# Performance work log

Measured on AMD Instinct MI355X. Metric: run time of the kernel, lower is better.

Reference implementation:

```python
import jax, jax.numpy as jnp
import numpy as np
from jax import lax

B, N, NUM_CLS_P1, MASK_DIM, PH, PW = 2, 19248, 81, 32, 138, 138
MAX_OUT, MAX_CLS_OUT = 300, 100
IOU_THR, SCORE_THR, SIGMA = 0.5, 0.3, 0.5


def setup_inputs() -> dict:
    key = jax.random.key(0)
    k1, k2, k3, k4, k5 = jax.random.split(key, 5)
    pred_offset = jax.random.normal(k1, (B, N, 4), jnp.float32) * 0.05
    # scale logits so softmax produces a realistic spread of scores above 0.3
    pred_cls = jax.random.normal(k2, (B, N, NUM_CLS_P1), jnp.float32) * 3.0
    pred_mask_coef = jax.random.normal(k3, (B, N, MASK_DIM), jnp.float32)
    pr = jax.random.uniform(k4, (N, 4), jnp.float32)
    ctr, wh = pr[:, :2], 0.05 + 0.2 * pr[:, 2:]
    priors = jnp.concatenate([ctr - wh / 2, ctr + wh / 2], axis=-1)  # [N,4] y1x1y2x2-ish
    proto_out = jax.random.normal(k5, (B, PH, PW, MASK_DIM), jnp.float32)
    return dict(pred_offset=pred_offset, pred_cls=pred_cls,
                pred_mask_coef=pred_mask_coef, priors=priors, proto_out=proto_out)


def _corners(b):
    # TF NMS normalizes unordered corners with min/max
    y1 = jnp.minimum(b[..., 0], b[..., 2]); y2 = jnp.maximum(b[..., 0], b[..., 2])
    x1 = jnp.minimum(b[..., 1], b[..., 3]); x2 = jnp.maximum(b[..., 1], b[..., 3])
    return y1, x1, y2, x2


def soft_nms(boxes, scores):
    # boxes [N,4], scores [N] -> (idx [K], score [K], valid [K]); valid is a prefix mask
    y1, x1, y2, x2 = _corners(boxes)
    area = (y2 - y1) * (x2 - x1)

    def step(s, _):
        i = jnp.argmax(s)
        sc = s[i]
        valid = sc > SCORE_THR  # TF NMSv5 selects strictly above score_threshold
        iy1 = jnp.maximum(y1, y1[i]); ix1 = jnp.maximum(x1, x1[i])
        iy2 = jnp.minimum(y2, y2[i]); ix2 = jnp.minimum(x2, x2[i])
        inter = jnp.maximum(iy2 - iy1, 0.0) * jnp.maximum(ix2 - ix1, 0.0)
        union = area + area[i] - inter
        iou = jnp.where((area > 0.0) & (area[i] > 0.0),
                        inter / jnp.where(union > 0.0, union, 1.0), 0.0)
        # Gaussian soft suppression below hard IoU threshold, hard zero above (TF semantics)
        w = jnp.where(iou <= IOU_THR, jnp.exp((-0.5 / SIGMA) * iou * iou), 0.0)
        s_new = (s * w).at[i].set(-jnp.inf)
        s_next = jnp.where(valid, s_new, s)  # freeze once below threshold (selection stops)
        return s_next, (i, sc, valid)

    _, (idx, sc, valid) = lax.scan(step, scores, None, length=MAX_CLS_OUT)
    return idx, sc, valid


def detect_one(boxes, cls_scores, coefs, proto):
    # boxes [N,4], cls_scores [N,C], coefs [N,D], proto [H,W,D]
    C = cls_scores.shape[1]
    idx, sc, valid = jax.vmap(lambda s: soft_nms(boxes, s))(cls_scores.T)  # [C,K]
    vf = valid.astype(boxes.dtype)
    sel_boxes = boxes[idx] * vf[..., None]                          # [C,K,4]
    sel_coefs = coefs[idx] * vf[..., None]                          # [C,K,D]
    sel_scores = jnp.where(valid, sc, 0.0)                          # [C,K]
    sel_classes = jnp.where(valid, jnp.arange(1, C + 1, dtype=boxes.dtype)[:, None], 0.0)
    flat_scores = sel_scores.reshape(-1)
    order = jnp.argsort(-flat_scores)[:MAX_OUT]
    out_boxes = sel_boxes.reshape(-1, 4)[order]
    out_coefs = sel_coefs.reshape(-1, sel_coefs.shape[-1])[order]
    out_classes = sel_classes.reshape(-1)[order]
    out_scores = flat_scores[order]
    masks = jax.nn.sigmoid(jnp.einsum('hwd,kd->khw', proto, out_coefs))  # [K,H,W]
    return out_boxes, out_classes, out_scores, masks


def reference(pred_offset, pred_cls, pred_mask_coef, priors, proto_out):
    box_decode = pred_offset + priors[None]                          # [B,N,4]
    probs = jax.nn.softmax(pred_cls, axis=-1)[..., 1:]               # drop background [B,N,C]
    boxes_o, classes_o, scores_o, masks_o = jax.vmap(detect_one)(
        box_decode, probs, pred_mask_coef, proto_out)
    # original slices the (C*K)-sized buffer with [:max_output_size] -> always 300 when any prior passes
    any_pass = jnp.any(jnp.max(probs, axis=-1) > SCORE_THR, axis=-1)
    num_det = jnp.where(any_pass, MAX_OUT, 0).astype(jnp.int32)
    return boxes_o, classes_o, scores_o, masks_o, num_det
```

## Files before the change

kernel.cpp:

```cpp
#include <hip/hip_runtime.h>
#include <cstdint>
#include <cstddef>

#define B_ 2
#define N_ 19248
#define NCLSP1_ 81
#define NCLS_ 80
#define MAXK_ 100
#define MAXOUT_ 300
#define PH_ 138
#define PW_ 138
#define PHW_ (PH_*PW_)
#define MD_ 32
#define NBC_ (B_*NCLS_)
#define CAP_ 768
#define SCORE_THR_ 0.3f
#define IOU_THR_ 0.5f

#define OUT_BOXES 0
#define OUT_CLS   2400
#define OUT_SCR   3000
#define OUT_MASKS 3600
#define OUT_NDET  11430000
#define OUT_HEAD  3600

#define OFF_CURSORS 0
#define POOLSZ      (NBC_*CAP_)
#define OFF_PS      2576
#define OFF_PY1     (OFF_PS  + POOLSZ)
#define OFF_PX1     (OFF_PY1 + POOLSZ)
#define OFF_PY2     (OFF_PX1 + POOLSZ)
#define OFF_PX2     (OFF_PY2 + POOLSZ)
#define OFF_PA      (OFF_PX2 + POOLSZ)
#define OFF_PIDX    (OFF_PA  + POOLSZ)
#define OFF_NSCORE  (OFF_PIDX + POOLSZ)
#define OFF_NANCH   (OFF_NSCORE + NBC_*MAXK_)
#define OFF_SELC    (OFF_NANCH + NBC_*MAXK_)

__device__ __forceinline__ float wave_max_f32(float x) {
    int v = __float_as_int(x);
    int t;
    #define DPPMAX(ctrl, rm, bm) \
        t = __builtin_amdgcn_update_dpp(v, v, ctrl, rm, bm, false); \
        v = __float_as_int(fmaxf(__int_as_float(v), __int_as_float(t)));
    DPPMAX(0x111, 0xF, 0xF)
    DPPMAX(0x112, 0xF, 0xF)
    DPPMAX(0x114, 0xF, 0xE)
    DPPMAX(0x118, 0xF, 0xC)
    DPPMAX(0x142, 0xA, 0xF)
    DPPMAX(0x143, 0xC, 0xF)
    #undef DPPMAX
    return __int_as_float(__builtin_amdgcn_readlane(v, 63));
}

__device__ __forceinline__ float wave_sum_f32(float x) {
    int v = __float_as_int(x);
    int t;
    #define DPPSUM(ctrl, rm, bm) \
        t = __builtin_amdgcn_update_dpp(v, v, ctrl, rm, bm, false); \
        v = __float_as_int(__int_as_float(v) + __int_as_float(t));
    DPPSUM(0x111, 0xF, 0xF)
    DPPSUM(0x112, 0xF, 0xF)
    DPPSUM(0x114, 0xF, 0xE)
    DPPSUM(0x118, 0xF, 0xC)
    DPPSUM(0x142, 0xA, 0xF)
    DPPSUM(0x143, 0xC, 0xF)
    #undef DPPSUM
    return __int_as_float(__builtin_amdgcn_readlane(v, 63));
}

__device__ __forceinline__ float readlane_f(float v, int l) {
    return __int_as_float(__builtin_amdgcn_readlane(__float_as_int(v), l));
}

__global__ __launch_bounds__(256) void k_fused(const float* __restrict__ cls,
        const float* __restrict__ off4, const float* __restrict__ priors,
        int* __restrict__ cursors,
        float* __restrict__ ps, float* __restrict__ py1, float* __restrict__ px1,
        float* __restrict__ py2, float* __restrict__ px2, float* __restrict__ pa,
        int* __restrict__ pidx) {
    int wid = (blockIdx.x * 256 + threadIdx.x) >> 6;
    int lane = threadIdx.x & 63;
    if (wid >= B_ * N_) return;
    int b = wid / N_;
    int n = wid - b * N_;
    const float* x = cls + (size_t)wid * NCLSP1_;
    float v1 = x[lane];
    float v2 = (lane <= 16) ? x[lane + 64] : -INFINITY;
    float mx = wave_max_f32(fmaxf(v1, v2));
    float e1 = __expf(v1 - mx);
    float e2 = (lane <= 16) ? __expf(v2 - mx) : 0.f;
    float sum = wave_sum_f32(e1 + e2);
    float p1 = e1 / sum;
    float p2 = e2 / sum;
    bool q1 = (lane >= 1) && (p1 > SCORE_THR_);
    bool q2 = (lane <= 16) && (p2 > SCORE_THR_);
    if (q1 | q2) {
        float4 o  = *(const float4*)(off4 + (size_t)wid * 4);
        float4 pr = *(const float4*)(priors + (size_t)n * 4);
        float d0 = o.x + pr.x, d1 = o.y + pr.y, d2 = o.z + pr.z, d3 = o.w + pr.w;
        float y1 = fminf(d0, d2), y2 = fmaxf(d0, d2);
        float x1 = fminf(d1, d3), x2 = fmaxf(d1, d3);
        float ar = (y2 - y1) * (x2 - x1);
        if (q1) {
            int bc = b * NCLS_ + (lane - 1);
            int pos = atomicAdd(&cursors[bc * 16], 1);
            if (pos < CAP_) {
                int o0 = bc * CAP_ + pos;
                ps[o0] = p1; py1[o0] = y1; px1[o0] = x1;
                py2[o0] = y2; px2[o0] = x2; pa[o0] = ar; pidx[o0] = n;
            }
        }
        if (q2) {
            int bc = b * NCLS_ + (lane + 63);
            int pos = atomicAdd(&cursors[bc * 16], 1);
            if (pos < CAP_) {
                int o0 = bc * CAP_ + pos;
                ps[o0] = p2; py1[o0] = y1; px1[o0] = x1;
                py2[o0] = y2; px2[o0] = x2; pa[o0] = ar; pidx[o0] = n;
            }
        }
    }
}

template<int J>
__device__ __forceinline__ void nms_reg(int bc, int M, int lane,
        const float* __restrict__ ps, const float* __restrict__ py1,
        const float* __restrict__ px1, const float* __restrict__ py2,
        const float* __restrict__ px2, const float* __restrict__ pa,
        const int* __restrict__ pidx,
        float* __restrict__ nscore, int* __restrict__ nanchor) {
    int base = bc * CAP_;
    float s[J], y1[J], x1[J], y2[J], x2[J], a[J];
    int pid[J];
    #pragma unroll
    for (int j = 0; j < J; j++) {
        int m = lane + 64 * j;
        bool in = (m < M);
        s[j]  = in ? ps[base + m]  : 0.f;
        y1[j] = in ? py1[base + m] : 0.f;
        x1[j] = in ? px1[base + m] : 0.f;
        y2[j] = in ? py2[base + m] : 0.f;
        x2[j] = in ? px2[base + m] : 0.f;
        a[j]  = in ? pa[base + m]  : 0.f;
        pid[j] = in ? pidx[base + m] : 0;
    }
    float lm = s[0];
    #pragma unroll
    for (int j = 1; j < J; j++) lm = fmaxf(lm, s[j]);
    for (int k = 0; k < MAXK_; k++) {
        float maxv = wave_max_f32(lm);
        if (!(maxv > SCORE_THR_)) break;
        unsigned long long bb[J];
        #pragma unroll
        for (int j = 0; j < J; j++) bb[j] = __ballot(s[j] == maxv);
        int bsel = 0;
        #pragma unroll
        for (int j = J - 1; j >= 0; j--) if (bb[j]) bsel = 64 * j + (__ffsll((long long)bb[j]) - 1);
        int lsel = bsel & 63;
        float ty1, tx1, ty2, tx2; int tpd;
        if (J == 1) {
            ty1 = y1[0]; tx1 = x1[0]; ty2 = y2[0]; tx2 = x2[0]; tpd = pid[0];
        } else {
            int jsel = bsel >> 6;
            ty1 = y1[0]; tx1 = x1[0]; ty2 = y2[0]; tx2 = x2[0]; tpd = pid[0];
            #pragma unroll
            for (int j = 1; j < J; j++) {
                if (j == jsel) { ty1 = y1[j]; tx1 = x1[j]; ty2 = y2[j]; tx2 = x2[j]; tpd = pid[j]; }
            }
        }
        float by1 = readlane_f(ty1, lsel);
        float bx1 = readlane_f(tx1, lsel);
        float by2 = readlane_f(ty2, lsel);
        float bx2 = readlane_f(tx2, lsel);
        int   bpd = __builtin_amdgcn_readlane(tpd, lsel);
        float ba  = (by2 - by1) * (bx2 - bx1);
        if (lane == 0) {
            nscore[bc * MAXK_ + k] = maxv;
            nanchor[bc * MAXK_ + k] = bpd;
        }
        lm = 0.f;
        #pragma unroll
        for (int j = 0; j < J; j++) {
            float iy1 = fmaxf(y1[j], by1), ix1 = fmaxf(x1[j], bx1);
            float iy2 = fminf(y2[j], by2), ix2 = fminf(x2[j], bx2);
            float inter = fmaxf(iy2 - iy1, 0.f) * fmaxf(ix2 - ix1, 0.f);
            float un = a[j] + ba - inter;
            float iou = inter * __builtin_amdgcn_rcpf(un);
            float w = (iou <= IOU_THR_) ? __expf(-iou * iou) : 0.f;
            s[j] = s[j] * w;
            lm = fmaxf(lm, s[j]);
        }
    }
}

__device__ void nms_glb(int bc, int M, int lane,
        float* __restrict__ ps, float* __restrict__ py1, float* __restrict__ px1,
        float* __restrict__ py2, float* __restrict__ px2, float* __restrict__ pa,
        const int* __restrict__ pidx,
        float* __restrict__ nscore, int* __restrict__ nanchor) {
    int base = bc * CAP_;
    float* S = ps + base; float* Y1 = py1 + base; float* X1 = px1 + base;
    float* Y2 = py2 + base; float* X2 = px2 + base; float* A = pa + base;
    float bvv = -INFINITY; int bii = 0x7FFFFFFF;
    for (int m = lane; m < M; m += 64) { float v = S[m]; if (v > bvv) { bvv = v; bii = m; } }
    #pragma unroll
    for (int off = 32; off > 0; off >>= 1) {
        float ov = __shfl_xor(bvv, off);
        int   oi = __shfl_xor(bii, off);
        if (ov > bvv || (ov == bvv && oi < bii)) { bvv = ov; bii = oi; }
    }
    for (int k = 0; k < MAXK_; k++) {
        float val = bvv;
        if (!(val > SCORE_THR_)) break;
        int bsel = bii;
        if (lane == 0) {
            nscore[bc * MAXK_ + k] = val;
            nanchor[bc * MAXK_ + k] = pidx[base + bsel];
        }
        float by1 = Y1[bsel], bx1 = X1[bsel], by2 = Y2[bsel], bx2 = X2[bsel], ba = A[bsel];
        bvv = -INFINITY; bii = 0x7FFFFFFF;
        for (int m = lane; m < M; m += 64) {
            float s0 = S[m];
            float ns;
            if (s0 == -INFINITY) {
                ns = s0;
            } else {
                float iy1 = fmaxf(Y1[m], by1), ix1 = fmaxf(X1[m], bx1);
                float iy2 = fminf(Y2[m], by2), ix2 = fminf(X2[m], bx2);
                float inter = fmaxf(iy2 - iy1, 0.f) * fmaxf(ix2 - ix1, 0.f);
                float am = A[m];
                float un = am + ba - inter;
                float iou = (am > 0.f && ba > 0.f) ? inter / (un > 0.f ? un : 1.f) : 0.f;
                float w = (iou <= IOU_THR_) ? __expf(-iou * iou) : 0.f;
                ns = (m == bsel) ? -INFINITY : s0 * w;
                S[m] = ns;
            }
            if (ns > bvv) { bvv = ns; bii = m; }
        }
        #pragma unroll
        for (int off = 32; off > 0; off >>= 1) {
            float ov = __shfl_xor(bvv, off);
            int   oi = __shfl_xor(bii, off);
            if (ov > bvv || (ov == bvv && oi < bii)) { bvv = ov; bii = oi; }
        }
    }
}

__global__ __launch_bounds__(64) void k_nms(const int* __restrict__ cursors,
        float* __restrict__ ps, float* __restrict__ py1, float* __restrict__ px1,
        float* __restrict__ py2, float* __restrict__ px2, float* __restrict__ pa,
        const int* __restrict__ pidx,
        float* __restrict__ nscore, int* __restrict__ nanchor,
        float* __restrict__ out_head, float* __restrict__ selc) {
    int bc = blockIdx.x;
    int lane = threadIdx.x & 63;
    int M = cursors[bc * 16];
    if (M > CAP_) M = CAP_;
    for (int k = lane; k < MAXK_; k += 64) { nscore[bc * MAXK_ + k] = 0.f; nanchor[bc * MAXK_ + k] = 0; }
    for (int i = bc * 64 + lane; i < OUT_HEAD + B_ * MAXOUT_ * MD_; i += NBC_ * 64) {
        if (i < OUT_HEAD) out_head[i] = 0.f;
        else selc[i - OUT_HEAD] = 0.f;
    }
    if (M <= 0) return;
    if (M <= 64)  { nms_reg<1>(bc, M, lane, ps, py1, px1, py2, px2, pa, pidx, nscore, nanchor); return; }
    if (M <= 128) { nms_reg<2>(bc, M, lane, ps, py1, px1, py2, px2, pa, pidx, nscore, nanchor); return; }
    if (M <= 192) { nms_reg<3>(bc, M, lane, ps, py1, px1, py2, px2, pa, pidx, nscore, nanchor); return; }
    if (M <= 256) { nms_reg<4>(bc, M, lane, ps, py1, px1, py2, px2, pa, pidx, nscore, nanchor); return; }
    if (M <= 512) { nms_reg<8>(bc, M, lane, ps, py1, px1, py2, px2, pa, pidx, nscore, nanchor); return; }
    nms_glb(bc, M, lane, ps, py1, px1, py2, px2, pa, pidx, nscore, nanchor);
}

__global__ __launch_bounds__(1024) void k_rank(const float* __restrict__ nscore,
        const int* __restrict__ nanchor,
        const float* __restrict__ off4, const float* __restrict__ priors,
        const float* __restrict__ coef, float* __restrict__ out, float* __restrict__ selc) {
    int b = blockIdx.y;
    int tid = threadIdx.x;
    __shared__ unsigned long long key[NCLS_ * MAXK_];
    __shared__ int anyf;
    if (tid == 0) anyf = 0;
    for (int i = tid; i < NCLS_ * MAXK_; i += 1024) {
        float s = nscore[b * (NCLS_ * MAXK_) + i];
        key[i] = ((unsigned long long)__float_as_uint(s) << 32)
               | (unsigned)(0xFFFFFFFFu - (unsigned)i);
    }
    __syncthreads();
    if (tid < NCLS_ && (unsigned)(key[tid * MAXK_] >> 32) != 0u) anyf = 1;
    __syncthreads();
    if (blockIdx.x == 0 && tid == 0) out[OUT_NDET + b] = anyf ? (float)MAXOUT_ : 0.f;

    int i = blockIdx.x * 1000 + tid;
    if (tid >= 1000 || i >= NCLS_ * MAXK_) return;
    unsigned long long mykey = key[i];
    if ((unsigned)(mykey >> 32) == 0u) return;

    int rank = 0;
    #pragma unroll
    for (int cg = 0; cg < NCLS_; cg += 8) {
        int lo0=0,lo1=0,lo2=0,lo3=0,lo4=0,lo5=0,lo6=0,lo7=0;
        int hi0=MAXK_,hi1=MAXK_,hi2=MAXK_,hi3=MAXK_,hi4=MAXK_,hi5=MAXK_,hi6=MAXK_,hi7=MAXK_;
        #pragma unroll
        for (int it = 0; it < 7; it++) {
            #define BSTEP(u, lo, hi) { \
                int mid = (lo + hi) >> 1; \
                if (lo < hi) { \
                    unsigned long long v = key[(cg + u) * MAXK_ + mid]; \
                    if (v > mykey) lo = mid + 1; else hi = mid; \
                } }
            BSTEP(0, lo0, hi0) BSTEP(1, lo1, hi1) BSTEP(2, lo2, hi2) BSTEP(3, lo3, hi3)
            BSTEP(4, lo4, hi4) BSTEP(5, lo5, hi5) BSTEP(6, lo6, hi6) BSTEP(7, lo7, hi7)
            #undef BSTEP
        }
        rank += lo0+lo1+lo2+lo3+lo4+lo5+lo6+lo7;
    }
    if (rank >= MAXOUT_) return;

    float s = __uint_as_float((unsigned)(mykey >> 32));
    int c = i / MAXK_;
    int anchor = nanchor[b * (NCLS_ * MAXK_) + i];
    out[OUT_SCR + b * MAXOUT_ + rank] = s;
    out[OUT_CLS + b * MAXOUT_ + rank] = (float)(c + 1);
    size_t gb = (size_t)b * N_ + anchor;
    #pragma unroll
    for (int t = 0; t < 4; t++) {
        float v = off4[gb * 4 + t] + priors[(size_t)anchor * 4 + t];
        out[OUT_BOXES + ((size_t)b * MAXOUT_ + rank) * 4 + t] = v;
    }
    #pragma unroll
    for (int d = 0; d < MD_; d++) {
        selc[((size_t)b * MAXOUT_ + rank) * MD_ + d] = coef[gb * MD_ + d];
    }
}

#define KCHUNK 75
__global__ __launch_bounds__(256) void k_masks(const float* __restrict__ proto,
        const float* __restrict__ selc, float* __restrict__ om) {
    int b = blockIdx.z;
    int k0 = blockIdx.y * KCHUNK;
    int p = blockIdx.x * 256 + threadIdx.x;
    __shared__ float cf[KCHUNK * MD_];
    for (int i = threadIdx.x; i < KCHUNK * MD_; i += 256)
        cf[i] = selc[((size_t)b * MAXOUT_ + k0) * MD_ + i];
    __syncthreads();
    if (p >= PHW_) return;
    const float4* pp = (const float4*)(proto + ((size_t)b * PHW_ + p) * MD_);
    float4 pr[8];
    #pragma unroll
    for (int i = 0; i < 8; i++) pr[i] = pp[i];
    float* ob = om + ((size_t)b * MAXOUT_ + k0) * PHW_ + p;
    for (int kk = 0; kk < KCHUNK; kk++) {
        const float4* cv = (const float4*)(cf + kk * MD_);
        float acc = 0.f;
        #pragma unroll
        for (int i = 0; i < 8; i++) {
            float4 c = cv[i];
            acc += pr[i].x * c.x + pr[i].y * c.y + pr[i].z * c.z + pr[i].w * c.w;
        }
        ob[(size_t)kk * PHW_] = 1.f / (1.f + __expf(-acc));
    }
}

extern "C" void kernel_launch(void* const* d_in, const int* in_sizes, int n_in,
                              void* d_out, int out_size, void* d_ws, size_t ws_size,
                              hipStream_t stream) {
    const float* pred_offset = (const float*)d_in[0];
    const float* pred_cls    = (const float*)d_in[1];
    const float* pred_coef   = (const float*)d_in[2];
    const float* priors      = (const float*)d_in[3];
    const float* proto       = (const float*)d_in[4];
    float* out = (float*)d_out;
    float* ws  = (float*)d_ws;
    int*   wsi = (int*)d_ws;

    int*   cursors = wsi + OFF_CURSORS;
    float* ps      = ws  + OFF_PS;
    float* py1     = ws  + OFF_PY1;
    float* px1     = ws  + OFF_PX1;
    float* py2     = ws  + OFF_PY2;
    float* px2     = ws  + OFF_PX2;
    float* pa      = ws  + OFF_PA;
    int*   pidx    = wsi + OFF_PIDX;
    float* nscore  = ws  + OFF_NSCORE;
    int*   nanchor = wsi + OFF_NANCH;
    float* selc    = ws  + OFF_SELC;

    hipMemsetAsync(d_ws, 0, 2560 * 4, stream);

    k_fused<<<(B_ * N_ * 64 + 255) / 256, 256, 0, stream>>>(pred_cls, pred_offset, priors,
            cursors, ps, py1, px1, py2, px2, pa, pidx);
    k_nms<<<NBC_, 64, 0, stream>>>(cursors, ps, py1, px1, py2, px2, pa, pidx,
                                   nscore, nanchor, out, selc);
    k_rank<<<dim3(8, B_), 1024, 0, stream>>>(nscore, nanchor,
                                             pred_offset, priors, pred_coef, out, selc);
    k_masks<<<dim3((PHW_ + 255) / 256, MAXOUT_ / KCHUNK, B_), 256, 0, stream>>>(proto, selc, out + OUT_MASKS);
}
```

Baseline: 144.6 us.

## Merge all four stages into one cooperative persistent kernel with grid syncs

Replaces the four separate launches (scoring/compaction, per-class NMS, ranking, mask GEMM) with a single cooperative kernel on a fixed 256-block grid, using grid.sync between stages. The rank stage no longer stages keys in shared memory and instead builds them on the fly from global nscore. Detection counts now come from per-batch flags set during NMS. The aim is to remove launch gaps and inter-kernel overhead, at the cost of less parallelism in the compaction and mask stages, a serialized NMS stage running one wave per block, and global-memory binary searches.

```diff
diff --git a/kernel.cpp b/kernel.cpp
--- a/kernel.cpp
+++ b/kernel.cpp
@@ -1,6 +1,9 @@
 #include <hip/hip_runtime.h>
+#include <hip/hip_cooperative_groups.h>
 #include <cstdint>
 #include <cstddef>
+
+namespace cg = cooperative_groups;
 
 #define B_ 2
 #define N_ 19248
@@ -16,6 +19,9 @@
 #define CAP_ 768
 #define SCORE_THR_ 0.3f
 #define IOU_THR_ 0.5f
+#define KCHUNK 75
+#define GRID_ 256
+#define NTILE 608
 
 #define OUT_BOXES 0
 #define OUT_CLS   2400
@@ -25,6 +31,7 @@
 #define OUT_HEAD  3600
 
 #define OFF_CURSORS 0
+#define OFF_BFLAG   2560
 #define POOLSZ      (NBC_*CAP_)
 #define OFF_PS      2576
 #define OFF_PY1     (OFF_PS  + POOLSZ)
@@ -71,56 +78,6 @@
 
 __device__ __forceinline__ float readlane_f(float v, int l) {
     return __int_as_float(__builtin_amdgcn_readlane(__float_as_int(v), l));
-}
-
-__global__ __launch_bounds__(256) void k_fused(const float* __restrict__ cls,
-        const float* __restrict__ off4, const float* __restrict__ priors,
-        int* __restrict__ cursors,
-        float* __restrict__ ps, float* __restrict__ py1, float* __restrict__ px1,
-        float* __restrict__ py2, float* __restrict__ px2, float* __restrict__ pa,
-        int* __restrict__ pidx) {
-    int wid = (blockIdx.x * 256 + threadIdx.x) >> 6;
-    int lane = threadIdx.x & 63;
-    if (wid >= B_ * N_) return;
-    int b = wid / N_;
-    int n = wid - b * N_;
-    const float* x = cls + (size_t)wid * NCLSP1_;
-    float v1 = x[lane];
-    float v2 = (lane <= 16) ? x[lane + 64] : -INFINITY;
-    float mx = wave_max_f32(fmaxf(v1, v2));
-    float e1 = __expf(v1 - mx);
-    float e2 = (lane <= 16) ? __expf(v2 - mx) : 0.f;
-    float sum = wave_sum_f32(e1 + e2);
-    float p1 = e1 / sum;
-    float p2 = e2 / sum;
-    bool q1 = (lane >= 1) && (p1 > SCORE_THR_);
-    bool q2 = (lane <= 16) && (p2 > SCORE_THR_);
-    if (q1 | q2) {
-        float4 o  = *(const float4*)(off4 + (size_t)wid * 4);
-        float4 pr = *(const float4*)(priors + (size_t)n * 4);
-        float d0 = o.x + pr.x, d1 = o.y + pr.y, d2 = o.z + pr.z, d3 = o.w + pr.w;
-        float y1 = fminf(d0, d2), y2 = fmaxf(d0, d2);
-        float x1 = fminf(d1, d3), x2 = fmaxf(d1, d3);
-        float ar = (y2 - y1) * (x2 - x1);
-        if (q1) {
-            int bc = b * NCLS_ + (lane - 1);
-            int pos = atomicAdd(&cursors[bc * 16], 1);
-            if (pos < CAP_) {
-                int o0 = bc * CAP_ + pos;
-                ps[o0] = p1; py1[o0] = y1; px1[o0] = x1;
-                py2[o0] = y2; px2[o0] = x2; pa[o0] = ar; pidx[o0] = n;
-            }
-        }
-        if (q2) {
-            int bc = b * NCLS_ + (lane + 63);
-            int pos = atomicAdd(&cursors[bc * 16], 1);
-            if (pos < CAP_) {
-                int o0 = bc * CAP_ + pos;
-                ps[o0] = p2; py1[o0] = y1; px1[o0] = x1;
-                py2[o0] = y2; px2[o0] = x2; pa[o0] = ar; pidx[o0] = n;
-            }
-        }
-    }
 }
 
 template<int J>
@@ -247,117 +204,165 @@
     }
 }
 
-__global__ __launch_bounds__(64) void k_nms(const int* __restrict__ cursors,
+__global__ __launch_bounds__(256, 2) void k_all(
+        const float* __restrict__ cls, const float* __restrict__ off4,
+        const float* __restrict__ priors, const float* __restrict__ coef,
+        const float* __restrict__ proto,
+        int* __restrict__ cursors, int* __restrict__ bflags,
         float* __restrict__ ps, float* __restrict__ py1, float* __restrict__ px1,
         float* __restrict__ py2, float* __restrict__ px2, float* __restrict__ pa,
-        const int* __restrict__ pidx,
-        float* __restrict__ nscore, int* __restrict__ nanchor,
-        float* __restrict__ out_head, float* __restrict__ selc) {
-    int bc = blockIdx.x;
-    int lane = threadIdx.x & 63;
-    int M = cursors[bc * 16];
-    if (M > CAP_) M = CAP_;
-    for (int k = lane; k < MAXK_; k += 64) { nscore[bc * MAXK_ + k] = 0.f; nanchor[bc * MAXK_ + k] = 0; }
-    for (int i = bc * 64 + lane; i < OUT_HEAD + B_ * MAXOUT_ * MD_; i += NBC_ * 64) {
-        if (i < OUT_HEAD) out_head[i] = 0.f;
-        else selc[i - OUT_HEAD] = 0.f;
-    }
-    if (M <= 0) return;
-    if (M <= 64)  { nms_reg<1>(bc, M, lane, ps, py1, px1, py2, px2, pa, pidx, nscore, nanchor); return; }
-    if (M <= 128) { nms_reg<2>(bc, M, lane, ps, py1, px1, py2, px2, pa, pidx, nscore, nanchor); return; }
-    if (M <= 192) { nms_reg<3>(bc, M, lane, ps, py1, px1, py2, px2, pa, pidx, nscore, nanchor); return; }
-    if (M <= 256) { nms_reg<4>(bc, M, lane, ps, py1, px1, py2, px2, pa, pidx, nscore, nanchor); return; }
-    if (M <= 512) { nms_reg<8>(bc, M, lane, ps, py1, px1, py2, px2, pa, pidx, nscore, nanchor); return; }
-    nms_glb(bc, M, lane, ps, py1, px1, py2, px2, pa, pidx, nscore, nanchor);
-}
-
-__global__ __launch_bounds__(1024) void k_rank(const float* __restrict__ nscore,
-        const int* __restrict__ nanchor,
-        const float* __restrict__ off4, const float* __restrict__ priors,
-        const float* __restrict__ coef, float* __restrict__ out, float* __restrict__ selc) {
-    int b = blockIdx.y;
-    int tid = threadIdx.x;
-    __shared__ unsigned long long key[NCLS_ * MAXK_];
-    __shared__ int anyf;
-    if (tid == 0) anyf = 0;
-    for (int i = tid; i < NCLS_ * MAXK_; i += 1024) {
-        float s = nscore[b * (NCLS_ * MAXK_) + i];
-        key[i] = ((unsigned long long)__float_as_uint(s) << 32)
-               | (unsigned)(0xFFFFFFFFu - (unsigned)i);
-    }
-    __syncthreads();
-    if (tid < NCLS_ && (unsigned)(key[tid * MAXK_] >> 32) != 0u) anyf = 1;
-    __syncthreads();
-    if (blockIdx.x == 0 && tid == 0) out[OUT_NDET + b] = anyf ? (float)MAXOUT_ : 0.f;
-
-    int i = blockIdx.x * 1000 + tid;
-    if (tid >= 1000 || i >= NCLS_ * MAXK_) return;
-    unsigned long long mykey = key[i];
-    if ((unsigned)(mykey >> 32) == 0u) return;
-
-    int rank = 0;
-    #pragma unroll
-    for (int cg = 0; cg < NCLS_; cg += 8) {
-        int lo0=0,lo1=0,lo2=0,lo3=0,lo4=0,lo5=0,lo6=0,lo7=0;
-        int hi0=MAXK_,hi1=MAXK_,hi2=MAXK_,hi3=MAXK_,hi4=MAXK_,hi5=MAXK_,hi6=MAXK_,hi7=MAXK_;
-        #pragma unroll
-        for (int it = 0; it < 7; it++) {
-            #define BSTEP(u, lo, hi) { \
-                int mid = (lo + hi) >> 1; \
-                if (lo < hi) { \
-                    unsigned long long v = key[(cg + u) * MAXK_ + mid]; \
-                    if (v > mykey) lo = mid + 1; else hi = mid; \
-                } }
-            BSTEP(0, lo0, hi0) BSTEP(1, lo1, hi1) BSTEP(2, lo2, hi2) BSTEP(3, lo3, hi3)
-            BSTEP(4, lo4, hi4) BSTEP(5, lo5, hi5) BSTEP(6, lo6, hi6) BSTEP(7, lo7, hi7)
-            #undef BSTEP
-        }
-        rank += lo0+lo1+lo2+lo3+lo4+lo5+lo6+lo7;
-    }
-    if (rank >= MAXOUT_) return;
-
-    float s = __uint_as_float((unsigned)(mykey >> 32));
-    int c = i / MAXK_;
-    int anchor = nanchor[b * (NCLS_ * MAXK_) + i];
-    out[OUT_SCR + b * MAXOUT_ + rank] = s;
-    out[OUT_CLS + b * MAXOUT_ + rank] = (float)(c + 1);
-    size_t gb = (size_t)b * N_ + anchor;
-    #pragma unroll
-    for (int t = 0; t < 4; t++) {
-        float v = off4[gb * 4 + t] + priors[(size_t)anchor * 4 + t];
-        out[OUT_BOXES + ((size_t)b * MAXOUT_ + rank) * 4 + t] = v;
-    }
-    #pragma unroll
-    for (int d = 0; d < MD_; d++) {
-        selc[((size_t)b * MAXOUT_ + rank) * MD_ + d] = coef[gb * MD_ + d];
-    }
-}
-
-#define KCHUNK 75
-__global__ __launch_bounds__(256) void k_masks(const float* __restrict__ proto,
-        const float* __restrict__ selc, float* __restrict__ om) {
-    int b = blockIdx.z;
-    int k0 = blockIdx.y * KCHUNK;
-    int p = blockIdx.x * 256 + threadIdx.x;
-    __shared__ float cf[KCHUNK * MD_];
-    for (int i = threadIdx.x; i < KCHUNK * MD_; i += 256)
-        cf[i] = selc[((size_t)b * MAXOUT_ + k0) * MD_ + i];
-    __syncthreads();
-    if (p >= PHW_) return;
-    const float4* pp = (const float4*)(proto + ((size_t)b * PHW_ + p) * MD_);
-    float4 pr[8];
-    #pragma unroll
-    for (int i = 0; i < 8; i++) pr[i] = pp[i];
-    float* ob = om + ((size_t)b * MAXOUT_ + k0) * PHW_ + p;
-    for (int kk = 0; kk < KCHUNK; kk++) {
-        const float4* cv = (const float4*)(cf + kk * MD_);
-        float acc = 0.f;
-        #pragma unroll
-        for (int i = 0; i < 8; i++) {
-            float4 c = cv[i];
-            acc += pr[i].x * c.x + pr[i].y * c.y + pr[i].z * c.z + pr[i].w * c.w;
-        }
-        ob[(size_t)kk * PHW_] = 1.f / (1.f + __expf(-acc));
+        int* __restrict__ pidx, float* __restrict__ nscore, int* __restrict__ nanchor,
+        float* __restrict__ selc, float* __restrict__ out) {
+    cg::grid_group grid = cg::this_grid();
+    const int tid = threadIdx.x;
+    const int bid = blockIdx.x;
+    const int lane = tid & 63;
+    const int nb = gridDim.x;
+
+    for (int wid = bid * 4 + (tid >> 6); wid < B_ * N_; wid += nb * 4) {
+        int b = wid / N_;
+        int n = wid - b * N_;
+        const float* x = cls + (size_t)wid * NCLSP1_;
+        float v1 = x[lane];
+        float v2 = (lane <= 16) ? x[lane + 64] : -INFINITY;
+        float mx = wave_max_f32(fmaxf(v1, v2));
+        float e1 = __expf(v1 - mx);
+        float e2 = (lane <= 16) ? __expf(v2 - mx) : 0.f;
+        float sum = wave_sum_f32(e1 + e2);
+        float p1 = e1 / sum;
+        float p2 = e2 / sum;
+        bool q1 = (lane >= 1) && (p1 > SCORE_THR_);
+        bool q2 = (lane <= 16) && (p2 > SCORE_THR_);
+        if (q1 | q2) {
+            float4 o  = *(const float4*)(off4 + (size_t)wid * 4);
+            float4 pr = *(const float4*)(priors + (size_t)n * 4);
+            float d0 = o.x + pr.x, d1 = o.y + pr.y, d2 = o.z + pr.z, d3 = o.w + pr.w;
+            float y1 = fminf(d0, d2), y2 = fmaxf(d0, d2);
+            float x1 = fminf(d1, d3), x2 = fmaxf(d1, d3);
+            float ar = (y2 - y1) * (x2 - x1);
+            if (q1) {
+                int bc = b * NCLS_ + (lane - 1);
+                int pos = atomicAdd(&cursors[bc * 16], 1);
+                if (pos < CAP_) {
+                    int o0 = bc * CAP_ + pos;
+                    ps[o0] = p1; py1[o0] = y1; px1[o0] = x1;
+                    py2[o0] = y2; px2[o0] = x2; pa[o0] = ar; pidx[o0] = n;
+                }
+            }
+            if (q2) {
+                int bc = b * NCLS_ + (lane + 63);
+                int pos = atomicAdd(&cursors[bc * 16], 1);
+                if (pos < CAP_) {
+                    int o0 = bc * CAP_ + pos;
+                    ps[o0] = p2; py1[o0] = y1; px1[o0] = x1;
+                    py2[o0] = y2; px2[o0] = x2; pa[o0] = ar; pidx[o0] = n;
+                }
+            }
+        }
+    }
+    grid.sync();
+
+    for (int i = bid * 256 + tid; i < OUT_HEAD + B_ * MAXOUT_ * MD_; i += nb * 256) {
+        if (i < OUT_HEAD) out[i] = 0.f; else selc[i - OUT_HEAD] = 0.f;
+    }
+    if (bid < NBC_ && (tid >> 6) == 0) {
+        int bc = bid;
+        int M = cursors[bc * 16];
+        if (M > CAP_) M = CAP_;
+        for (int k = lane; k < MAXK_; k += 64) { nscore[bc * MAXK_ + k] = 0.f; nanchor[bc * MAXK_ + k] = 0; }
+        if (M > 0) {
+            if (lane == 0) bflags[bc / NCLS_] = 1;
+            if (M <= 64)       nms_reg<1>(bc, M, lane, ps, py1, px1, py2, px2, pa, pidx, nscore, nanchor);
+            else if (M <= 128) nms_reg<2>(bc, M, lane, ps, py1, px1, py2, px2, pa, pidx, nscore, nanchor);
+            else if (M <= 192) nms_reg<3>(bc, M, lane, ps, py1, px1, py2, px2, pa, pidx, nscore, nanchor);
+            else if (M <= 256) nms_reg<4>(bc, M, lane, ps, py1, px1, py2, px2, pa, pidx, nscore, nanchor);
+            else if (M <= 512) nms_reg<8>(bc, M, lane, ps, py1, px1, py2, px2, pa, pidx, nscore, nanchor);
+            else               nms_glb(bc, M, lane, ps, py1, px1, py2, px2, pa, pidx, nscore, nanchor);
+        }
+    }
+    grid.sync();
+
+    for (int gth = bid * 256 + tid; gth < B_ * NCLS_ * MAXK_; gth += nb * 256) {
+        if (gth < B_) out[OUT_NDET + gth] = bflags[gth] ? (float)MAXOUT_ : 0.f;
+        int b = gth / (NCLS_ * MAXK_);
+        int i = gth - b * (NCLS_ * MAXK_);
+        const float* nsb = nscore + (size_t)b * (NCLS_ * MAXK_);
+        float sv = nsb[i];
+        if (sv != 0.f) {
+            unsigned long long mykey = ((unsigned long long)__float_as_uint(sv) << 32)
+                                     | (unsigned)(0xFFFFFFFFu - (unsigned)i);
+            #define KEYAT(ii) ((((unsigned long long)__float_as_uint(nsb[ii])) << 32) \
+                               | (unsigned)(0xFFFFFFFFu - (unsigned)(ii)))
+            int rank = 0;
+            #pragma unroll
+            for (int cgp = 0; cgp < NCLS_; cgp += 8) {
+                int lo0=0,lo1=0,lo2=0,lo3=0,lo4=0,lo5=0,lo6=0,lo7=0;
+                int hi0=MAXK_,hi1=MAXK_,hi2=MAXK_,hi3=MAXK_,hi4=MAXK_,hi5=MAXK_,hi6=MAXK_,hi7=MAXK_;
+                #pragma unroll
+                for (int it = 0; it < 7; it++) {
+                    #define BSTEP(u, lo, hi) { \
+                        int mid = (lo + hi) >> 1; \
+                        if (lo < hi) { \
+                            unsigned long long v = KEYAT((cgp + u) * MAXK_ + mid); \
+                            if (v > mykey) lo = mid + 1; else hi = mid; \
+                        } }
+                    BSTEP(0, lo0, hi0) BSTEP(1, lo1, hi1) BSTEP(2, lo2, hi2) BSTEP(3, lo3, hi3)
+                    BSTEP(4, lo4, hi4) BSTEP(5, lo5, hi5) BSTEP(6, lo6, hi6) BSTEP(7, lo7, hi7)
+                    #undef BSTEP
+                }
+                rank += lo0+lo1+lo2+lo3+lo4+lo5+lo6+lo7;
+            }
+            #undef KEYAT
+            if (rank < MAXOUT_) {
+                int c = i / MAXK_;
+                int anchor = nanchor[(size_t)b * (NCLS_ * MAXK_) + i];
+                out[OUT_SCR + b * MAXOUT_ + rank] = sv;
+                out[OUT_CLS + b * MAXOUT_ + rank] = (float)(c + 1);
+                size_t gb = (size_t)b * N_ + anchor;
+                #pragma unroll
+                for (int t = 0; t < 4; t++) {
+                    float v = off4[gb * 4 + t] + priors[(size_t)anchor * 4 + t];
+                    out[OUT_BOXES + ((size_t)b * MAXOUT_ + rank) * 4 + t] = v;
+                }
+                #pragma unroll
+                for (int d = 0; d < MD_; d++) {
+                    selc[((size_t)b * MAXOUT_ + rank) * MD_ + d] = coef[gb * MD_ + d];
+                }
+            }
+        }
+    }
+    grid.sync();
+
+    {
+        __shared__ float cf[KCHUNK * MD_];
+        for (int tile = bid; tile < NTILE; tile += nb) {
+            __syncthreads();
+            int pb = tile % 76;
+            int kc = (tile / 76) & 3;
+            int b  = tile / 304;
+            int k0 = kc * KCHUNK;
+            for (int i = tid; i < KCHUNK * MD_; i += 256)
+                cf[i] = selc[((size_t)b * MAXOUT_ + k0) * MD_ + i];
+            __syncthreads();
+            int p = pb * 256 + tid;
+            if (p < PHW_) {
+                const float4* pp = (const float4*)(proto + ((size_t)b * PHW_ + p) * MD_);
+                float4 pr[8];
+                #pragma unroll
+                for (int i = 0; i < 8; i++) pr[i] = pp[i];
+                float* ob = out + OUT_MASKS + ((size_t)b * MAXOUT_ + k0) * PHW_ + p;
+                for (int kk = 0; kk < KCHUNK; kk++) {
+                    const float4* cv = (const float4*)(cf + kk * MD_);
+                    float acc = 0.f;
+                    #pragma unroll
+                    for (int i = 0; i < 8; i++) {
+                        float4 c = cv[i];
+                        acc += pr[i].x * c.x + pr[i].y * c.y + pr[i].z * c.z + pr[i].w * c.w;
+                    }
+                    ob[(size_t)kk * PHW_] = 1.f / (1.f + __expf(-acc));
+                }
+            }
+        }
     }
 }
 
@@ -374,6 +379,7 @@
     int*   wsi = (int*)d_ws;
 
     int*   cursors = wsi + OFF_CURSORS;
+    int*   bflags  = wsi + OFF_BFLAG;
     float* ps      = ws  + OFF_PS;
     float* py1     = ws  + OFF_PY1;
     float* px1     = ws  + OFF_PX1;
@@ -385,13 +391,15 @@
     int*   nanchor = wsi + OFF_NANCH;
     float* selc    = ws  + OFF_SELC;
 
-    hipMemsetAsync(d_ws, 0, 2560 * 4, stream);
-
-    k_fused<<<(B_ * N_ * 64 + 255) / 256, 256, 0, stream>>>(pred_cls, pred_offset, priors,
-            cursors, ps, py1, px1, py2, px2, pa, pidx);
-    k_nms<<<NBC_, 64, 0, stream>>>(cursors, ps, py1, px1, py2, px2, pa, pidx,
-                                   nscore, nanchor, out, selc);
-    k_rank<<<dim3(8, B_), 1024, 0, stream>>>(nscore, nanchor,
-                                             pred_offset, priors, pred_coef, out, selc);
-    k_masks<<<dim3((PHW_ + 255) / 256, MAXOUT_ / KCHUNK, B_), 256, 0, stream>>>(proto, selc, out + OUT_MASKS);
-}
+    hipMemsetAsync(d_ws, 0, (size_t)OFF_PS * 4, stream);
+
+    void* args[] = {
+        (void*)&pred_cls, (void*)&pred_offset, (void*)&priors, (void*)&pred_coef,
+        (void*)&proto,
+        (void*)&cursors, (void*)&bflags,
+        (void*)&ps, (void*)&py1, (void*)&px1, (void*)&py2, (void*)&px2, (void*)&pa,
+        (void*)&pidx, (void*)&nscore, (void*)&nanchor,
+        (void*)&selc, (void*)&out
+    };
+    hipLaunchCooperativeKernel((const void*)k_all, dim3(GRID_), dim3(256), args, 0, stream);
+}
```

Result: slower. 283.9 us (+96.3%).
